# Performance work log

Hardware: AMD Instinct MI355X
Metric: run time of the kernel (lower is better)

The kernel has to match this reference:

```python
import jax, jax.numpy as jnp
import numpy as np
from jax.scipy.special import logsumexp

N_STATES = 512
VOCAB = 10000
BATCH = 64
T_MAX = 1024


def setup_inputs() -> dict:
    key = jax.random.key(0)
    k1, k2, k3, k4, k5 = jax.random.split(key, 5)
    x = jax.random.randint(k1, (BATCH, T_MAX), 0, VOCAB)
    T = jax.random.randint(k2, (BATCH,), 1, T_MAX + 1)  # lengths in [1, T_max]
    priors = jax.random.normal(k3, (N_STATES,), dtype=jnp.float32)
    trans = jax.random.normal(k4, (N_STATES, N_STATES), dtype=jnp.float32)
    emit = jax.random.normal(k5, (N_STATES, VOCAB), dtype=jnp.float32)
    return {"x": x, "T": T, "priors": priors, "trans": trans, "emit": emit}


def reference(x, T, priors, trans, emit):
    # x: (B, Tmax) int, T: (B,) int lengths
    log_pi = jax.nn.log_softmax(priors)            # (N,)
    log_T = jax.nn.log_softmax(trans, axis=0)      # (N, N), columns normalized (dim=0 in torch)
    log_E = jax.nn.log_softmax(emit, axis=1)       # (N, M)

    em = log_E.T[x]                                # (B, Tmax, N) emission log-probs per timestep
    la0 = em[:, 0] + log_pi                        # (B, N)

    def step(la_prev, em_t):
        # out[b, j] = logsumexp_k log_T[j, k] + la_prev[b, k]
        la_new = em_t + logsumexp(log_T[None, :, :] + la_prev[:, None, :], axis=2)
        return la_new, logsumexp(la_new, axis=1)   # carry, per-step log-sum over states

    _, sums = jax.lax.scan(step, la0, jnp.moveaxis(em[:, 1:], 1, 0))  # sums: (Tmax-1, B)
    log_sums = jnp.concatenate([logsumexp(la0, axis=1)[None, :], sums], axis=0)  # (Tmax, B)

    idx = jnp.clip(T, 1, x.shape[1]) - 1           # (B,)
    log_probs = jnp.take_along_axis(log_sums.T, idx[:, None], axis=1)  # (B, 1)
    return log_probs
```

## Files before the change

### kernel.cpp

```cpp
#include <hip/hip_runtime.h>
#include <hip/hip_bf16.h>


typedef unsigned long long u64;
typedef unsigned int u32;
typedef unsigned short u16;
using f32x4 = __attribute__((ext_vector_type(4))) float;
using i32x8 = __attribute__((ext_vector_type(8))) int;

#define N_ST 512
#define VOCAB 10000
#define BATCH 64
#define T_MAX 1024

#define WS_EB       0
#define WS_GB       10240000
#define WS_A8       20480000
#define WS_ROWLSE   20742144
#define WS_COLLSE   20744192
#define WS_PINORM   20746240

static __device__ __forceinline__ float bf16f(u16 h) {
    return __uint_as_float((u32)h << 16);
}
static __device__ __forceinline__ u16 bf16enc(float f) {
    u32 u = __float_as_uint(f);
    return (u16)((u + 0x7fffu + ((u >> 16) & 1u)) >> 16);
}

static __device__ __forceinline__ float dec8(u32 b) {
    float nrm = __uint_as_float((b << 20) + 0x3C000000u);
    float dnm = (float)b * 0x1p-9f;
    return b >= 8u ? nrm : dnm;
}

static __device__ __forceinline__ u32 enc_e4m3(float f) {
    if (!(f > 0.f)) return 0u;
    unsigned u = __float_as_uint(f);
    int e = (int)((u >> 23) & 0xff) - 127;
    unsigned m = u & 0x7fffffu;
    if (e > 8 || (e == 8 && m >= 0x700000u)) return 0x7eu;
    if (e >= -6) {
        unsigned mant = m >> 20;
        unsigned rest = m & 0xfffffu;
        if (rest > 0x80000u || (rest == 0x80000u && (mant & 1u))) mant++;
        unsigned r = ((unsigned)(e + 7) << 3) + mant;
        return r > 0x7eu ? 0x7eu : r;
    }
    if (e < -10) return 0u;
    unsigned full = 0x800000u | m;
    int shift = 23 - (e + 9);
    unsigned r = full >> shift;
    unsigned rem = full & ((1u << shift) - 1u);
    unsigned half = 1u << (shift - 1);
    if (rem > half || (rem == half && (r & 1u))) r++;
    return r;
}

template <bool HI>
static __device__ __forceinline__ u32 cvtpk2(float a, float b, u32 old) {
#if __has_builtin(__builtin_amdgcn_cvt_pk_fp8_f32)
    return (u32)__builtin_amdgcn_cvt_pk_fp8_f32(a, b, (int)old, HI);
#else
    unsigned v = enc_e4m3(a) | (enc_e4m3(b) << 8);
    return HI ? ((old & 0x0000ffffu) | (v << 16)) : ((old & 0xffff0000u) | v);
#endif
}

__global__ __launch_bounds__(256) void k_row_lse(const float* __restrict__ emit,
                                                 float* __restrict__ rowLSE) {
    const int n = blockIdx.x;
    const float* row = emit + (size_t)n * VOCAB;
    __shared__ float redm[4], reds[4];
    const int tid = threadIdx.x, lane = tid & 63, wid = tid >> 6;

    float m = -INFINITY;
    for (int i = tid; i < VOCAB; i += 256) m = fmaxf(m, row[i]);
    #pragma unroll
    for (int o = 32; o; o >>= 1) m = fmaxf(m, __shfl_down(m, o));
    if (lane == 0) redm[wid] = m;
    __syncthreads();
    if (tid == 0) redm[0] = fmaxf(fmaxf(redm[0], redm[1]), fmaxf(redm[2], redm[3]));
    __syncthreads();
    m = redm[0];

    float s = 0.f;
    for (int i = tid; i < VOCAB; i += 256) s += __expf(row[i] - m);
    #pragma unroll
    for (int o = 32; o; o >>= 1) s += __shfl_down(s, o);
    if (lane == 0) reds[wid] = s;
    __syncthreads();
    if (tid == 0) rowLSE[n] = m + __logf(reds[0] + reds[1] + reds[2] + reds[3]);
}

__global__ __launch_bounds__(256) void k_expEmitT(const float* __restrict__ emit,
                                                  const float* __restrict__ rowLSE,
                                                  u16* __restrict__ Eb) {
    const size_t gid = (size_t)blockIdx.x * 256 + threadIdx.x;
    const int m = (int)(gid >> 9);
    const int n = (int)(gid & 511);
    Eb[gid] = bf16enc(__expf(emit[(size_t)n * VOCAB + m] - rowLSE[n]));
}

__global__ __launch_bounds__(256) void k_col_lse(const float* __restrict__ trans,
                                                 float* __restrict__ colLSE) {
    const int k = blockIdx.x;
    const int tid = threadIdx.x, lane = tid & 63, wid = tid >> 6;
    __shared__ float redm[4], reds[4];

    float a = trans[(size_t)tid * N_ST + k];
    float b = trans[(size_t)(tid + 256) * N_ST + k];
    float m = fmaxf(a, b);
    #pragma unroll
    for (int o = 32; o; o >>= 1) m = fmaxf(m, __shfl_down(m, o));
    if (lane == 0) redm[wid] = m;
    __syncthreads();
    if (tid == 0) redm[0] = fmaxf(fmaxf(redm[0], redm[1]), fmaxf(redm[2], redm[3]));
    __syncthreads();
    m = redm[0];

    float s = __expf(a - m) + __expf(b - m);
    #pragma unroll
    for (int o = 32; o; o >>= 1) s += __shfl_down(s, o);
    if (lane == 0) reds[wid] = s;
    __syncthreads();
    if (tid == 0) colLSE[k] = m + __logf(reds[0] + reds[1] + reds[2] + reds[3]);
}

__global__ __launch_bounds__(64) void k_packA_fp8(const float* __restrict__ trans,
                                                  const float* __restrict__ colLSE,
                                                  u32* __restrict__ A8) {
    const int f = blockIdx.x;
    const int l = threadIdx.x;
    const int w = f >> 4, ks = (f >> 2) & 3, jt = f & 3;
    const int j = w * 64 + jt * 16 + (l & 15);
    const int k0 = ks * 128 + (l >> 4) * 32;
    u32 dw[8];
    #pragma unroll
    for (int d = 0; d < 8; ++d) {
        float a0 = 256.0f * __expf(trans[(size_t)j * N_ST + k0 + 4 * d + 0] - colLSE[k0 + 4 * d + 0]);
        float a1 = 256.0f * __expf(trans[(size_t)j * N_ST + k0 + 4 * d + 1] - colLSE[k0 + 4 * d + 1]);
        float a2 = 256.0f * __expf(trans[(size_t)j * N_ST + k0 + 4 * d + 2] - colLSE[k0 + 4 * d + 2]);
        float a3 = 256.0f * __expf(trans[(size_t)j * N_ST + k0 + 4 * d + 3] - colLSE[k0 + 4 * d + 3]);
        u32 pk = cvtpk2<false>(a0, a1, 0u);
        dw[d] = cvtpk2<true>(a2, a3, pk);
    }
    u32* dst = A8 + (size_t)f * 512 + l * 8;
    *(uint4*)dst       = make_uint4(dw[0], dw[1], dw[2], dw[3]);
    *(uint4*)(dst + 4) = make_uint4(dw[4], dw[5], dw[6], dw[7]);
}

__global__ __launch_bounds__(512) void k_pinorm(const float* __restrict__ priors,
                                                float* __restrict__ pinorm) {
    const int j = threadIdx.x, lane = j & 63, wid = j >> 6;
    __shared__ float redm[8], reds[8];
    float v = priors[j];

    float m = v;
    #pragma unroll
    for (int o = 32; o; o >>= 1) m = fmaxf(m, __shfl_down(m, o));
    if (lane == 0) redm[wid] = m;
    __syncthreads();
    if (j == 0) {
        float r = redm[0];
        for (int i = 1; i < 8; ++i) r = fmaxf(r, redm[i]);
        redm[0] = r;
    }
    __syncthreads();
    m = redm[0];

    float s = __expf(v - m);
    #pragma unroll
    for (int o = 32; o; o >>= 1) s += __shfl_down(s, o);
    if (lane == 0) reds[wid] = s;
    __syncthreads();
    if (j == 0) {
        float r = 0.f;
        for (int i = 0; i < 8; ++i) r += reds[i];
        reds[0] = r;
    }
    __syncthreads();
    pinorm[j] = __expf(v - m) / reds[0];
}

__global__ __launch_bounds__(256) void k_G(const u16* __restrict__ Eb,
                                           const float* __restrict__ trans,
                                           const float* __restrict__ colLSE,
                                           u16* __restrict__ Gb) {
    __shared__ float Es[16][512];
    const int m0 = blockIdx.x * 16;
    const int tid = threadIdx.x;
    for (int idx = tid; idx < 16 * 512; idx += 256)
        Es[idx >> 9][idx & 511] = bf16f(Eb[(size_t)(m0 + (idx >> 9)) * 512 + (idx & 511)]);
    __syncthreads();

    const int k0 = tid, k1 = tid + 256;
    const float c0 = colLSE[k0], c1 = colLSE[k1];
    float acc0[16], acc1[16];
    #pragma unroll
    for (int mi = 0; mi < 16; ++mi) { acc0[mi] = 0.f; acc1[mi] = 0.f; }

    for (int j = 0; j < 512; ++j) {
        float a0 = __expf(trans[(size_t)j * N_ST + k0] - c0);
        float a1 = __expf(trans[(size_t)j * N_ST + k1] - c1);
        #pragma unroll
        for (int mi = 0; mi < 16; ++mi) {
            float e = Es[mi][j];
            acc0[mi] = fmaf(e, a0, acc0[mi]);
            acc1[mi] = fmaf(e, a1, acc1[mi]);
        }
    }
    #pragma unroll
    for (int mi = 0; mi < 16; ++mi) {
        Gb[(size_t)(m0 + mi) * N_ST + k0] = bf16enc(acc0[mi]);
        Gb[(size_t)(m0 + mi) * N_ST + k1] = bf16enc(acc1[mi]);
    }
}

#define UNIT_SCALES 0x7f7f7f7f

#define WG_BARRIER()                                        \
  {                                                         \
    asm volatile("s_waitcnt lgkmcnt(0)" ::: "memory");      \
    __builtin_amdgcn_s_barrier();                           \
    asm volatile("" ::: "memory");                          \
  }

#define STEP_BODY(EU, GU, EP, GP)                                               \
  {                                                                             \
    const int xpre = xnext;                                                     \
    GP = *(const uint4*)((const char*)Gb + ((size_t)xpre << 10) + (l << 4));    \
    _Pragma("unroll")                                                           \
    for (int jt = 0; jt < 4; ++jt)                                              \
      EP[jt] = *(const u64*)(Eb + (size_t)xpre * N_ST + wbase + jt * 16 + rbase); \
    xnext = xb[(t + 2 <= Tf) ? (t + 2) : Tf];                                   \
    const u64 vown = vq[p][l];                                                  \
    const u32* vbase = (const u32*)&vq[p][0];                                   \
                                             \
    i32x8 bq[4];                                                                \
    _Pragma("unroll")                                                           \
    for (int ks = 0; ks < 4; ++ks) {                                            \
      const uint4 b0 = *(const uint4*)(vbase + ks * 32 + grp * 8);              \
      const uint4 b1 = *(const uint4*)(vbase + ks * 32 + grp * 8 + 4);          \
      bq[ks] = i32x8{(int)b0.x, (int)b0.y, (int)b0.z, (int)b0.w,                \
                     (int)b1.x, (int)b1.y, (int)b1.z, (int)b1.w};               \
    }                                                                           \
                               \
    f32x4 aA0={0,0,0,0}, aA1={0,0,0,0}, aA2={0,0,0,0}, aA3={0,0,0,0};           \
    f32x4 aB0={0,0,0,0}, aB1={0,0,0,0}, aB2={0,0,0,0}, aB3={0,0,0,0};           \
    _Pragma("unroll")                                                           \
    for (int kk = 0; kk < 2; ++kk) {                                            \
      const int ksA = kk * 2, ksB = kk * 2 + 1;                                 \
      aA0 = __builtin_amdgcn_mfma_scale_f32_16x16x128_f8f6f4(                   \
                af[ksA * 4 + 0], bq[ksA], aA0, 0, 0, 0, UNIT_SCALES, 0, UNIT_SCALES); \
      aB0 = __builtin_amdgcn_mfma_scale_f32_16x16x128_f8f6f4(                   \
                af[ksB * 4 + 0], bq[ksB], aB0, 0, 0, 0, UNIT_SCALES, 0, UNIT_SCALES); \
      aA1 = __builtin_amdgcn_mfma_scale_f32_16x16x128_f8f6f4(                   \
                af[ksA * 4 + 1], bq[ksA], aA1, 0, 0, 0, UNIT_SCALES, 0, UNIT_SCALES); \
      aB1 = __builtin_amdgcn_mfma_scale_f32_16x16x128_f8f6f4(                   \
                af[ksB * 4 + 1], bq[ksB], aB1, 0, 0, 0, UNIT_SCALES, 0, UNIT_SCALES); \
      aA2 = __builtin_amdgcn_mfma_scale_f32_16x16x128_f8f6f4(                   \
                af[ksA * 4 + 2], bq[ksA], aA2, 0, 0, 0, UNIT_SCALES, 0, UNIT_SCALES); \
      aB2 = __builtin_amdgcn_mfma_scale_f32_16x16x128_f8f6f4(                   \
                af[ksB * 4 + 2], bq[ksB], aB2, 0, 0, 0, UNIT_SCALES, 0, UNIT_SCALES); \
      aA3 = __builtin_amdgcn_mfma_scale_f32_16x16x128_f8f6f4(                   \
                af[ksA * 4 + 3], bq[ksA], aA3, 0, 0, 0, UNIT_SCALES, 0, UNIT_SCALES); \
      aB3 = __builtin_amdgcn_mfma_scale_f32_16x16x128_f8f6f4(                   \
                af[ksB * 4 + 3], bq[ksB], aB3, 0, 0, 0, UNIT_SCALES, 0, UNIT_SCALES); \
    }                                                                           \
    float gv = 0.f;                                                             \
    {                                                                           \
      const u32 gw[4] = {GU.x, GU.y, GU.z, GU.w};                               \
      _Pragma("unroll")                                                         \
      for (int i = 0; i < 4; ++i) {                                             \
        float g0 = bf16f((u16)(gw[i] & 0xffffu));                               \
        float g1 = bf16f((u16)(gw[i] >> 16));                                   \
        float v0 = dec8((u32)(vown >> (16 * i)) & 0xffu);                       \
        float v1 = dec8((u32)(vown >> (16 * i + 8)) & 0xffu);                   \
        gv = fmaf(g0, v0, gv);                                                  \
        gv = fmaf(g1, v1, gv);                                                  \
      }                                                                         \
      _Pragma("unroll")                                                         \
      for (int o = 1; o <= 32; o <<= 1) gv += __shfl_xor(gv, o);                \
    }                                                                           \
    float wv2[16];                                                              \
    _Pragma("unroll")                                                           \
    for (int r = 0; r < 4; ++r) {                                               \
      wv2[0 + r]  = bf16f((u16)(EU[0] >> (16 * r))) * (aA0[r] + aB0[r]);        \
      wv2[4 + r]  = bf16f((u16)(EU[1] >> (16 * r))) * (aA1[r] + aB1[r]);        \
      wv2[8 + r]  = bf16f((u16)(EU[2] >> (16 * r))) * (aA2[r] + aB2[r]);        \
      wv2[12 + r] = bf16f((u16)(EU[3] >> (16 * r))) * (aA3[r] + aB3[r]);        \
    }                                                                           \
    if (t == Tf) {                                                              \
      float s2 = 0.f;                                                           \
      _Pragma("unroll")                                                         \
      for (int i = 0; i < 16; ++i) s2 += wv2[i];                                \
      s2 += __shfl_xor(s2, 16);                                                 \
      s2 += __shfl_xor(s2, 32);                                                 \
      if (l == 0) red[wid] = s2;                                                \
      __syncthreads();                                                          \
      const float Se = red[0] + red[1] + red[2] + red[3] +                      \
                       red[4] + red[5] + red[6] + red[7];                       \
      if (tid == 0) out[b] = L + __logf(Se) - (float)Tb * LN256;                \
    } else {                                                                    \
      L += __logf(gv);                                                          \
      const float sc = 1.0f / gv;                                               \
      if ((l & 15) == 0) {                                                      \
        u32* vw = (u32*)&vq[p ^ 1][0];                                          \
        _Pragma("unroll")                                                       \
        for (int jt = 0; jt < 4; ++jt) {                                        \
          u32 pk = cvtpk2<false>(wv2[jt * 4 + 0] * sc, wv2[jt * 4 + 1] * sc, 0u); \
          pk = cvtpk2<true>(wv2[jt * 4 + 2] * sc, wv2[jt * 4 + 3] * sc, pk);    \
          vw[(wbase >> 2) + jt * 4 + grp] = pk;                                 \
        }                                                                       \
      }                                                                         \
      WG_BARRIER();                                                             \
      p ^= 1;                                                                   \
    }                                                                           \
  }

__global__ __launch_bounds__(512, 2) void hmm_main(const int* __restrict__ x,
                                                   const int* __restrict__ T,
                                                   const u16* __restrict__ Eb,
                                                   const u32* __restrict__ A8,
                                                   const u16* __restrict__ Gb,
                                                   const float* __restrict__ pinorm,
                                                   float* __restrict__ out) {
    __shared__ u64 vq[2][64];
    __shared__ float red[8];
    const int b = blockIdx.x;
    const int tid = threadIdx.x;
    const int l = tid & 63;
    const int wid = tid >> 6;
    const int grp = l >> 4;
    const int wbase = wid * 64;
    const int rbase = grp * 4;
    const float LN256 = 5.545177444479562f;

    int Tb = T[b];
    Tb = Tb < 1 ? 1 : (Tb > T_MAX ? T_MAX : Tb);
    const int* xb = x + (size_t)b * T_MAX;

    i32x8 af[16];
    {
        const u32* ap = A8 + (size_t)wid * 16 * 512 + l * 8;
        #pragma unroll
        for (int i = 0; i < 16; ++i) {
            uint4 lo = *(const uint4*)(ap + (size_t)i * 512);
            uint4 hi = *(const uint4*)(ap + (size_t)i * 512 + 4);
            af[i] = i32x8{(int)lo.x, (int)lo.y, (int)lo.z, (int)lo.w,
                          (int)hi.x, (int)hi.y, (int)hi.z, (int)hi.w};
        }
    }

    const int x0 = xb[0];
    const int x1 = xb[1];
    u64 eA[4], eB[4];
    uint4 gA, gB;
    gA = *(const uint4*)((const char*)Gb + ((size_t)x1 << 10) + (l << 4));
    #pragma unroll
    for (int jt = 0; jt < 4; ++jt)
        eA[jt] = *(const u64*)(Eb + (size_t)x1 * N_ST + wbase + jt * 16 + rbase);

    float wv[16];
    float s = 0.f;
    #pragma unroll
    for (int jt = 0; jt < 4; ++jt) {
        u64 eraw = *(const u64*)(Eb + (size_t)x0 * N_ST + wbase + jt * 16 + rbase);
        #pragma unroll
        for (int r = 0; r < 4; ++r) {
            const int j = wbase + jt * 16 + rbase + r;
            float e = bf16f((u16)(eraw >> (16 * r)));
            float t0 = e * pinorm[j];
            wv[jt * 4 + r] = t0;
            s += t0;
        }
    }
    s += __shfl_xor(s, 16);
    s += __shfl_xor(s, 32);
    if (l == 0) red[wid] = s;
    __syncthreads();
    float S0 = red[0] + red[1] + red[2] + red[3] + red[4] + red[5] + red[6] + red[7];
    float L = __logf(S0);
    if (Tb == 1) {
        if (tid == 0) out[b] = L;
        return;
    }
    __syncthreads();
    {
        const float sc = 256.0f / S0;
        if ((l & 15) == 0) {
            u32* vw = (u32*)&vq[0][0];
            #pragma unroll
            for (int jt = 0; jt < 4; ++jt) {
                u32 pk = cvtpk2<false>(wv[jt * 4 + 0] * sc, wv[jt * 4 + 1] * sc, 0u);
                pk = cvtpk2<true>(wv[jt * 4 + 2] * sc, wv[jt * 4 + 3] * sc, pk);
                vw[(wbase >> 2) + jt * 4 + grp] = pk;
            }
        }
    }
    __syncthreads();

    const int Tf = Tb - 1;
    int p = 0;
    int xnext = xb[(2 <= Tf) ? 2 : Tf];
    for (int t = 1;;) {
        STEP_BODY(eA, gA, eB, gB)
        if (t == Tf) break;
        ++t;
        STEP_BODY(eB, gB, eA, gA)
        if (t == Tf) break;
        ++t;
    }
}

extern "C" void kernel_launch(void* const* d_in, const int* in_sizes, int n_in,
                              void* d_out, int out_size, void* d_ws, size_t ws_size,
                              hipStream_t stream) {
    const int*   x      = (const int*)d_in[0];
    const int*   T      = (const int*)d_in[1];
    const float* priors = (const float*)d_in[2];
    const float* trans  = (const float*)d_in[3];
    const float* emit   = (const float*)d_in[4];
    float* out = (float*)d_out;

    char* ws = (char*)d_ws;
    u16*   Eb     = (u16*)(ws + WS_EB);
    u16*   Gb     = (u16*)(ws + WS_GB);
    u32*   A8     = (u32*)(ws + WS_A8);
    float* rowLSE = (float*)(ws + WS_ROWLSE);
    float* colLSE = (float*)(ws + WS_COLLSE);
    float* pinorm = (float*)(ws + WS_PINORM);

    k_row_lse<<<N_ST, 256, 0, stream>>>(emit, rowLSE);
    k_expEmitT<<<(VOCAB * N_ST) / 256, 256, 0, stream>>>(emit, rowLSE, Eb);
    k_col_lse<<<N_ST, 256, 0, stream>>>(trans, colLSE);
    k_packA_fp8<<<128, 64, 0, stream>>>(trans, colLSE, A8);
    k_pinorm<<<1, 512, 0, stream>>>(priors, pinorm);
    k_G<<<VOCAB / 16, 256, 0, stream>>>(Eb, trans, colLSE, Gb);

    hmm_main<<<BATCH, 512, 0, stream>>>(x, T, Eb, A8, Gb, pinorm, out);
}
```

Measured before the change: 1.294 ms.

## Interleave two batch chains per workgroup sharing one barrier per step

Each workgroup now processes two sequences, interleaving their forward-recursion steps so that the MFMA and latency chains of one can overlap the other. Both chains share a single workgroup barrier per timestep, halving the barriers per sequence. The grid is halved to 32 blocks, and the shorter chain idles until the longer one finishes. This lowers parallelism across CUs and raises register pressure.

```diff
diff --git a/kernel.cpp b/kernel.cpp
--- a/kernel.cpp
+++ b/kernel.cpp
@@ -218,6 +218,7 @@
 }
 
 #define UNIT_SCALES 0x7f7f7f7f
+#define LN256 5.545177444479562f
 
 #define WG_BARRIER()                                        \
   {                                                         \
@@ -226,17 +227,16 @@
     asm volatile("" ::: "memory");                          \
   }
 
-#define STEP_BODY(EU, GU, EP, GP)                                               \
-  {                                                                             \
-    const int xpre = xnext;                                                     \
+#define CHAIN_PRE(SUF, EU, GU, EP, GP)                                          \
+  if (t <= Tf##SUF) {                                                           \
+    const int xpre = xnext##SUF;                                                \
     GP = *(const uint4*)((const char*)Gb + ((size_t)xpre << 10) + (l << 4));    \
     _Pragma("unroll")                                                           \
     for (int jt = 0; jt < 4; ++jt)                                              \
       EP[jt] = *(const u64*)(Eb + (size_t)xpre * N_ST + wbase + jt * 16 + rbase); \
-    xnext = xb[(t + 2 <= Tf) ? (t + 2) : Tf];                                   \
-    const u64 vown = vq[p][l];                                                  \
-    const u32* vbase = (const u32*)&vq[p][0];                                   \
-                                             \
+    xnext##SUF = xb##SUF[(t + 2 <= Tf##SUF) ? (t + 2) : Tf##SUF];               \
+    const u64 vown = vq##SUF[p][l];                                             \
+    const u32* vbase = (const u32*)&vq##SUF[p][0];                              \
     i32x8 bq[4];                                                                \
     _Pragma("unroll")                                                           \
     for (int ks = 0; ks < 4; ++ks) {                                            \
@@ -245,7 +245,6 @@
       bq[ks] = i32x8{(int)b0.x, (int)b0.y, (int)b0.z, (int)b0.w,                \
                      (int)b1.x, (int)b1.y, (int)b1.z, (int)b1.w};               \
     }                                                                           \
-                               \
     f32x4 aA0={0,0,0,0}, aA1={0,0,0,0}, aA2={0,0,0,0}, aA3={0,0,0,0};           \
     f32x4 aB0={0,0,0,0}, aB1={0,0,0,0}, aB2={0,0,0,0}, aB3={0,0,0,0};           \
     _Pragma("unroll")                                                           \
@@ -291,22 +290,18 @@
       wv2[8 + r]  = bf16f((u16)(EU[2] >> (16 * r))) * (aA2[r] + aB2[r]);        \
       wv2[12 + r] = bf16f((u16)(EU[3] >> (16 * r))) * (aA3[r] + aB3[r]);        \
     }                                                                           \
-    if (t == Tf) {                                                              \
+    if (t == Tf##SUF) {                                                         \
       float s2 = 0.f;                                                           \
       _Pragma("unroll")                                                         \
       for (int i = 0; i < 16; ++i) s2 += wv2[i];                                \
       s2 += __shfl_xor(s2, 16);                                                 \
       s2 += __shfl_xor(s2, 32);                                                 \
-      if (l == 0) red[wid] = s2;                                                \
-      __syncthreads();                                                          \
-      const float Se = red[0] + red[1] + red[2] + red[3] +                      \
-                       red[4] + red[5] + red[6] + red[7];                       \
-      if (tid == 0) out[b] = L + __logf(Se) - (float)Tb * LN256;                \
+      if (l == 0) redF##SUF[wid] = s2;                                          \
     } else {                                                                    \
-      L += __logf(gv);                                                          \
+      L##SUF += __logf(gv);                                                     \
       const float sc = 1.0f / gv;                                               \
       if ((l & 15) == 0) {                                                      \
-        u32* vw = (u32*)&vq[p ^ 1][0];                                          \
+        u32* vw = (u32*)&vq##SUF[p ^ 1][0];                                     \
         _Pragma("unroll")                                                       \
         for (int jt = 0; jt < 4; ++jt) {                                        \
           u32 pk = cvtpk2<false>(wv2[jt * 4 + 0] * sc, wv2[jt * 4 + 1] * sc, 0u); \
@@ -314,9 +309,23 @@
           vw[(wbase >> 2) + jt * 4 + grp] = pk;                                 \
         }                                                                       \
       }                                                                         \
-      WG_BARRIER();                                                             \
-      p ^= 1;                                                                   \
     }                                                                           \
+  }
+
+#define CHAIN_POST(SUF, CIDX)                                                   \
+  if (t == Tf##SUF && Tb##SUF > 1) {                                            \
+    const float Se = redF##SUF[0] + redF##SUF[1] + redF##SUF[2] + redF##SUF[3] +\
+                     redF##SUF[4] + redF##SUF[5] + redF##SUF[6] + redF##SUF[7]; \
+    if (tid == 0) out[CIDX] = L##SUF + __logf(Se) - (float)Tb##SUF * LN256;     \
+  }
+
+#define ITER(EU0, GU0, EP0, GP0, EU1, GU1, EP1, GP1)                            \
+  {                                                                             \
+    CHAIN_PRE(0, EU0, GU0, EP0, GP0)                                            \
+    CHAIN_PRE(1, EU1, GU1, EP1, GP1)                                            \
+    WG_BARRIER();                                                               \
+    CHAIN_POST(0, c0)                                                           \
+    CHAIN_POST(1, c1)                                                           \
   }
 
 __global__ __launch_bounds__(512, 2) void hmm_main(const int* __restrict__ x,
@@ -326,20 +335,26 @@
                                                    const u16* __restrict__ Gb,
                                                    const float* __restrict__ pinorm,
                                                    float* __restrict__ out) {
-    __shared__ u64 vq[2][64];
-    __shared__ float red[8];
-    const int b = blockIdx.x;
+    __shared__ __align__(16) u64 vq0[2][64];
+    __shared__ __align__(16) u64 vq1[2][64];
+    __shared__ __align__(16) float redF0[8];
+    __shared__ __align__(16) float redF1[8];
+    const int c0 = 2 * blockIdx.x;
+    const int c1 = 2 * blockIdx.x + 1;
     const int tid = threadIdx.x;
     const int l = tid & 63;
     const int wid = tid >> 6;
     const int grp = l >> 4;
     const int wbase = wid * 64;
     const int rbase = grp * 4;
-    const float LN256 = 5.545177444479562f;
-
-    int Tb = T[b];
-    Tb = Tb < 1 ? 1 : (Tb > T_MAX ? T_MAX : Tb);
-    const int* xb = x + (size_t)b * T_MAX;
+
+    int Tb0 = T[c0]; Tb0 = Tb0 < 1 ? 1 : (Tb0 > T_MAX ? T_MAX : Tb0);
+    int Tb1 = T[c1]; Tb1 = Tb1 < 1 ? 1 : (Tb1 > T_MAX ? T_MAX : Tb1);
+    const int* xb0 = x + (size_t)c0 * T_MAX;
+    const int* xb1 = x + (size_t)c1 * T_MAX;
+    const int Tf0 = Tb0 - 1;
+    const int Tf1 = Tb1 - 1;
+    const int Tmax = Tf0 > Tf1 ? Tf0 : Tf1;
 
     i32x8 af[16];
     {
@@ -353,63 +368,84 @@
         }
     }
 
-    const int x0 = xb[0];
-    const int x1 = xb[1];
-    u64 eA[4], eB[4];
-    uint4 gA, gB;
-    gA = *(const uint4*)((const char*)Gb + ((size_t)x1 << 10) + (l << 4));
-    #pragma unroll
-    for (int jt = 0; jt < 4; ++jt)
-        eA[jt] = *(const u64*)(Eb + (size_t)x1 * N_ST + wbase + jt * 16 + rbase);
-
-    float wv[16];
-    float s = 0.f;
-    #pragma unroll
-    for (int jt = 0; jt < 4; ++jt) {
-        u64 eraw = *(const u64*)(Eb + (size_t)x0 * N_ST + wbase + jt * 16 + rbase);
+    u64 eA0[4], eB0[4], eA1[4], eB1[4];
+    uint4 gA0, gB0, gA1, gB1;
+    {
+        const int x10 = xb0[1];
+        const int x11 = xb1[1];
+        gA0 = *(const uint4*)((const char*)Gb + ((size_t)x10 << 10) + (l << 4));
+        gA1 = *(const uint4*)((const char*)Gb + ((size_t)x11 << 10) + (l << 4));
         #pragma unroll
-        for (int r = 0; r < 4; ++r) {
-            const int j = wbase + jt * 16 + rbase + r;
-            float e = bf16f((u16)(eraw >> (16 * r)));
-            float t0 = e * pinorm[j];
-            wv[jt * 4 + r] = t0;
-            s += t0;
+        for (int jt = 0; jt < 4; ++jt) {
+            eA0[jt] = *(const u64*)(Eb + (size_t)x10 * N_ST + wbase + jt * 16 + rbase);
+            eA1[jt] = *(const u64*)(Eb + (size_t)x11 * N_ST + wbase + jt * 16 + rbase);
         }
     }
-    s += __shfl_xor(s, 16);
-    s += __shfl_xor(s, 32);
-    if (l == 0) red[wid] = s;
-    __syncthreads();
-    float S0 = red[0] + red[1] + red[2] + red[3] + red[4] + red[5] + red[6] + red[7];
-    float L = __logf(S0);
-    if (Tb == 1) {
-        if (tid == 0) out[b] = L;
-        return;
-    }
-    __syncthreads();
+
+    float wv_0[16], wv_1[16];
     {
-        const float sc = 256.0f / S0;
+        const int x00 = xb0[0];
+        const int x01 = xb1[0];
+        float s0 = 0.f, s1 = 0.f;
+        #pragma unroll
+        for (int jt = 0; jt < 4; ++jt) {
+            u64 er0 = *(const u64*)(Eb + (size_t)x00 * N_ST + wbase + jt * 16 + rbase);
+            u64 er1 = *(const u64*)(Eb + (size_t)x01 * N_ST + wbase + jt * 16 + rbase);
+            #pragma unroll
+            for (int r = 0; r < 4; ++r) {
+                const int j = wbase + jt * 16 + rbase + r;
+                const float pj = pinorm[j];
+                float t0 = bf16f((u16)(er0 >> (16 * r))) * pj;
+                float t1 = bf16f((u16)(er1 >> (16 * r))) * pj;
+                wv_0[jt * 4 + r] = t0;  s0 += t0;
+                wv_1[jt * 4 + r] = t1;  s1 += t1;
+            }
+        }
+        s0 += __shfl_xor(s0, 16);  s0 += __shfl_xor(s0, 32);
+        s1 += __shfl_xor(s1, 16);  s1 += __shfl_xor(s1, 32);
+        if (l == 0) { redF0[wid] = s0; redF1[wid] = s1; }
+    }
+    __syncthreads();
+    const float S00 = redF0[0] + redF0[1] + redF0[2] + redF0[3] +
+                      redF0[4] + redF0[5] + redF0[6] + redF0[7];
+    const float S01 = redF1[0] + redF1[1] + redF1[2] + redF1[3] +
+                      redF1[4] + redF1[5] + redF1[6] + redF1[7];
+    float L0 = __logf(S00);
+    float L1 = __logf(S01);
+    if (Tb0 == 1 && tid == 0) out[c0] = L0;
+    if (Tb1 == 1 && tid == 0) out[c1] = L1;
+    if (Tmax == 0) return;
+    __syncthreads();
+    {
+        const float sc0 = 256.0f / S00;
+        const float sc1 = 256.0f / S01;
         if ((l & 15) == 0) {
-            u32* vw = (u32*)&vq[0][0];
+            u32* vw0 = (u32*)&vq0[0][0];
+            u32* vw1 = (u32*)&vq1[0][0];
             #pragma unroll
             for (int jt = 0; jt < 4; ++jt) {
-                u32 pk = cvtpk2<false>(wv[jt * 4 + 0] * sc, wv[jt * 4 + 1] * sc, 0u);
-                pk = cvtpk2<true>(wv[jt * 4 + 2] * sc, wv[jt * 4 + 3] * sc, pk);
-                vw[(wbase >> 2) + jt * 4 + grp] = pk;
+                u32 pk0 = cvtpk2<false>(wv_0[jt * 4 + 0] * sc0, wv_0[jt * 4 + 1] * sc0, 0u);
+                pk0 = cvtpk2<true>(wv_0[jt * 4 + 2] * sc0, wv_0[jt * 4 + 3] * sc0, pk0);
+                vw0[(wbase >> 2) + jt * 4 + grp] = pk0;
+                u32 pk1 = cvtpk2<false>(wv_1[jt * 4 + 0] * sc1, wv_1[jt * 4 + 1] * sc1, 0u);
+                pk1 = cvtpk2<true>(wv_1[jt * 4 + 2] * sc1, wv_1[jt * 4 + 3] * sc1, pk1);
+                vw1[(wbase >> 2) + jt * 4 + grp] = pk1;
             }
         }
     }
     __syncthreads();
 
-    const int Tf = Tb - 1;
     int p = 0;
-    int xnext = xb[(2 <= Tf) ? 2 : Tf];
+    int xnext0 = xb0[(2 <= Tf0) ? 2 : Tf0];
+    int xnext1 = xb1[(2 <= Tf1) ? 2 : Tf1];
     for (int t = 1;;) {
-        STEP_BODY(eA, gA, eB, gB)
-        if (t == Tf) break;
+        ITER(eA0, gA0, eB0, gB0, eA1, gA1, eB1, gB1)
+        p ^= 1;
+        if (t == Tmax) break;
         ++t;
-        STEP_BODY(eB, gB, eA, gA)
-        if (t == Tf) break;
+        ITER(eB0, gB0, eA0, gA0, eB1, gB1, eA1, gA1)
+        p ^= 1;
+        if (t == Tmax) break;
         ++t;
     }
 }
@@ -439,5 +475,5 @@
     k_pinorm<<<1, 512, 0, stream>>>(priors, pinorm);
     k_G<<<VOCAB / 16, 256, 0, stream>>>(Eb, trans, colLSE, Gb);
 
-    hmm_main<<<BATCH, 512, 0, stream>>>(x, T, Eb, A8, Gb, pinorm, out);
-}
+    hmm_main<<<BATCH / 2, 512, 0, stream>>>(x, T, Eb, A8, Gb, pinorm, out);
+}
```

After: 2.252 ms. 74.1% more time.

## Split HMM forward step across 16 waves of 32 states each

Applied to the files above, without the earlier changes.

Doubles the workgroup from 8 to 16 waves so each wave owns 32 output states instead of 64. Per-step MFMA work, A-fragment registers and emission loads per wave are halved, and the A8 packing is reorganized to match. This shortens the serial per-timestep critical path in the latency-bound recurrence. The cost is a barrier across twice as many waves, a 16-way reduction, and launch bounds of 1024 with one block per CU.

```diff
diff --git a/kernel.cpp b/kernel.cpp
--- a/kernel.cpp
+++ b/kernel.cpp
@@ -132,8 +132,8 @@
                                                   u32* __restrict__ A8) {
     const int f = blockIdx.x;
     const int l = threadIdx.x;
-    const int w = f >> 4, ks = (f >> 2) & 3, jt = f & 3;
-    const int j = w * 64 + jt * 16 + (l & 15);
+    const int w = f >> 3, ks = (f >> 1) & 3, jt = f & 1;
+    const int j = w * 32 + jt * 16 + (l & 15);
     const int k0 = ks * 128 + (l >> 4) * 32;
     u32 dw[8];
     #pragma unroll
@@ -218,6 +218,7 @@
 }
 
 #define UNIT_SCALES 0x7f7f7f7f
+#define LN256 5.545177444479562f
 
 #define WG_BARRIER()                                        \
   {                                                         \
@@ -231,42 +232,29 @@
     const int xpre = xnext;                                                     \
     GP = *(const uint4*)((const char*)Gb + ((size_t)xpre << 10) + (l << 4));    \
     _Pragma("unroll")                                                           \
-    for (int jt = 0; jt < 4; ++jt)                                              \
+    for (int jt = 0; jt < 2; ++jt)                                              \
       EP[jt] = *(const u64*)(Eb + (size_t)xpre * N_ST + wbase + jt * 16 + rbase); \
     xnext = xb[(t + 2 <= Tf) ? (t + 2) : Tf];                                   \
     const u64 vown = vq[p][l];                                                  \
-    const u32* vbase = (const u32*)&vq[p][0];                                   \
-                                             \
+    const char* vbase = (const char*)&vq[p][0];                                 \
     i32x8 bq[4];                                                                \
     _Pragma("unroll")                                                           \
-    for (int ks = 0; ks < 4; ++ks) {                                            \
-      const uint4 b0 = *(const uint4*)(vbase + ks * 32 + grp * 8);              \
-      const uint4 b1 = *(const uint4*)(vbase + ks * 32 + grp * 8 + 4);          \
-      bq[ks] = i32x8{(int)b0.x, (int)b0.y, (int)b0.z, (int)b0.w,                \
-                     (int)b1.x, (int)b1.y, (int)b1.z, (int)b1.w};               \
+    for (int ks = 0; ks < 4; ++ks)                                              \
+      bq[ks] = *(const i32x8*)(vbase + ks * 128 + grp * 32);                    \
+    f32x4 aA0={0,0,0,0}, aA1={0,0,0,0}, aB0={0,0,0,0}, aB1={0,0,0,0};           \
+    _Pragma("unroll")                                                           \
+    for (int ks = 0; ks < 2; ++ks) {                                            \
+      aA0 = __builtin_amdgcn_mfma_scale_f32_16x16x128_f8f6f4(                   \
+                af[ks * 2 + 0], bq[ks], aA0, 0, 0, 0, UNIT_SCALES, 0, UNIT_SCALES); \
+      aA1 = __builtin_amdgcn_mfma_scale_f32_16x16x128_f8f6f4(                   \
+                af[ks * 2 + 1], bq[ks], aA1, 0, 0, 0, UNIT_SCALES, 0, UNIT_SCALES); \
     }                                                                           \
-                               \
-    f32x4 aA0={0,0,0,0}, aA1={0,0,0,0}, aA2={0,0,0,0}, aA3={0,0,0,0};           \
-    f32x4 aB0={0,0,0,0}, aB1={0,0,0,0}, aB2={0,0,0,0}, aB3={0,0,0,0};           \
     _Pragma("unroll")                                                           \
-    for (int kk = 0; kk < 2; ++kk) {                                            \
-      const int ksA = kk * 2, ksB = kk * 2 + 1;                                 \
-      aA0 = __builtin_amdgcn_mfma_scale_f32_16x16x128_f8f6f4(                   \
-                af[ksA * 4 + 0], bq[ksA], aA0, 0, 0, 0, UNIT_SCALES, 0, UNIT_SCALES); \
+    for (int ks = 2; ks < 4; ++ks) {                                            \
       aB0 = __builtin_amdgcn_mfma_scale_f32_16x16x128_f8f6f4(                   \
-                af[ksB * 4 + 0], bq[ksB], aB0, 0, 0, 0, UNIT_SCALES, 0, UNIT_SCALES); \
-      aA1 = __builtin_amdgcn_mfma_scale_f32_16x16x128_f8f6f4(                   \
-                af[ksA * 4 + 1], bq[ksA], aA1, 0, 0, 0, UNIT_SCALES, 0, UNIT_SCALES); \
+                af[ks * 2 + 0], bq[ks], aB0, 0, 0, 0, UNIT_SCALES, 0, UNIT_SCALES); \
       aB1 = __builtin_amdgcn_mfma_scale_f32_16x16x128_f8f6f4(                   \
-                af[ksB * 4 + 1], bq[ksB], aB1, 0, 0, 0, UNIT_SCALES, 0, UNIT_SCALES); \
-      aA2 = __builtin_amdgcn_mfma_scale_f32_16x16x128_f8f6f4(                   \
-                af[ksA * 4 + 2], bq[ksA], aA2, 0, 0, 0, UNIT_SCALES, 0, UNIT_SCALES); \
-      aB2 = __builtin_amdgcn_mfma_scale_f32_16x16x128_f8f6f4(                   \
-                af[ksB * 4 + 2], bq[ksB], aB2, 0, 0, 0, UNIT_SCALES, 0, UNIT_SCALES); \
-      aA3 = __builtin_amdgcn_mfma_scale_f32_16x16x128_f8f6f4(                   \
-                af[ksA * 4 + 3], bq[ksA], aA3, 0, 0, 0, UNIT_SCALES, 0, UNIT_SCALES); \
-      aB3 = __builtin_amdgcn_mfma_scale_f32_16x16x128_f8f6f4(                   \
-                af[ksB * 4 + 3], bq[ksB], aB3, 0, 0, 0, UNIT_SCALES, 0, UNIT_SCALES); \
+                af[ks * 2 + 1], bq[ks], aB1, 0, 0, 0, UNIT_SCALES, 0, UNIT_SCALES); \
     }                                                                           \
     float gv = 0.f;                                                             \
     {                                                                           \
@@ -283,24 +271,23 @@
       _Pragma("unroll")                                                         \
       for (int o = 1; o <= 32; o <<= 1) gv += __shfl_xor(gv, o);                \
     }                                                                           \
-    float wv2[16];                                                              \
+    float wv2[8];                                                               \
     _Pragma("unroll")                                                           \
     for (int r = 0; r < 4; ++r) {                                               \
-      wv2[0 + r]  = bf16f((u16)(EU[0] >> (16 * r))) * (aA0[r] + aB0[r]);        \
-      wv2[4 + r]  = bf16f((u16)(EU[1] >> (16 * r))) * (aA1[r] + aB1[r]);        \
-      wv2[8 + r]  = bf16f((u16)(EU[2] >> (16 * r))) * (aA2[r] + aB2[r]);        \
-      wv2[12 + r] = bf16f((u16)(EU[3] >> (16 * r))) * (aA3[r] + aB3[r]);        \
+      wv2[0 + r] = bf16f((u16)(EU[0] >> (16 * r))) * (aA0[r] + aB0[r]);         \
+      wv2[4 + r] = bf16f((u16)(EU[1] >> (16 * r))) * (aA1[r] + aB1[r]);         \
     }                                                                           \
     if (t == Tf) {                                                              \
       float s2 = 0.f;                                                           \
       _Pragma("unroll")                                                         \
-      for (int i = 0; i < 16; ++i) s2 += wv2[i];                                \
+      for (int i = 0; i < 8; ++i) s2 += wv2[i];                                 \
       s2 += __shfl_xor(s2, 16);                                                 \
       s2 += __shfl_xor(s2, 32);                                                 \
-      if (l == 0) red[wid] = s2;                                                \
+      if (l == 0) redF[wid] = s2;                                               \
       __syncthreads();                                                          \
-      const float Se = red[0] + red[1] + red[2] + red[3] +                      \
-                       red[4] + red[5] + red[6] + red[7];                       \
+      float Se = 0.f;                                                           \
+      _Pragma("unroll")                                                         \
+      for (int i = 0; i < 16; ++i) Se += redF[i];                               \
       if (tid == 0) out[b] = L + __logf(Se) - (float)Tb * LN256;                \
     } else {                                                                    \
       L += __logf(gv);                                                          \
@@ -308,10 +295,10 @@
       if ((l & 15) == 0) {                                                      \
         u32* vw = (u32*)&vq[p ^ 1][0];                                          \
         _Pragma("unroll")                                                       \
-        for (int jt = 0; jt < 4; ++jt) {                                        \
+        for (int jt = 0; jt < 2; ++jt) {                                        \
           u32 pk = cvtpk2<false>(wv2[jt * 4 + 0] * sc, wv2[jt * 4 + 1] * sc, 0u); \
           pk = cvtpk2<true>(wv2[jt * 4 + 2] * sc, wv2[jt * 4 + 3] * sc, pk);    \
-          vw[(wbase >> 2) + jt * 4 + grp] = pk;                                 \
+          vw[wid * 8 + jt * 4 + grp] = pk;                                      \
         }                                                                       \
       }                                                                         \
       WG_BARRIER();                                                             \
@@ -319,53 +306,48 @@
     }                                                                           \
   }
 
-__global__ __launch_bounds__(512, 2) void hmm_main(const int* __restrict__ x,
-                                                   const int* __restrict__ T,
-                                                   const u16* __restrict__ Eb,
-                                                   const u32* __restrict__ A8,
-                                                   const u16* __restrict__ Gb,
-                                                   const float* __restrict__ pinorm,
-                                                   float* __restrict__ out) {
-    __shared__ u64 vq[2][64];
-    __shared__ float red[8];
+__global__ __launch_bounds__(1024, 1) void hmm_main(const int* __restrict__ x,
+                                                    const int* __restrict__ T,
+                                                    const u16* __restrict__ Eb,
+                                                    const u32* __restrict__ A8,
+                                                    const u16* __restrict__ Gb,
+                                                    const float* __restrict__ pinorm,
+                                                    float* __restrict__ out) {
+    __shared__ __align__(64) u64 vq[2][64];
+    __shared__ __align__(16) float redF[16];
     const int b = blockIdx.x;
     const int tid = threadIdx.x;
     const int l = tid & 63;
     const int wid = tid >> 6;
     const int grp = l >> 4;
-    const int wbase = wid * 64;
+    const int wbase = wid * 32;
     const int rbase = grp * 4;
-    const float LN256 = 5.545177444479562f;
 
     int Tb = T[b];
     Tb = Tb < 1 ? 1 : (Tb > T_MAX ? T_MAX : Tb);
     const int* xb = x + (size_t)b * T_MAX;
 
-    i32x8 af[16];
+    i32x8 af[8];
     {
-        const u32* ap = A8 + (size_t)wid * 16 * 512 + l * 8;
+        const u32* ap = A8 + (size_t)wid * 8 * 512 + l * 8;
         #pragma unroll
-        for (int i = 0; i < 16; ++i) {
-            uint4 lo = *(const uint4*)(ap + (size_t)i * 512);
-            uint4 hi = *(const uint4*)(ap + (size_t)i * 512 + 4);
-            af[i] = i32x8{(int)lo.x, (int)lo.y, (int)lo.z, (int)lo.w,
-                          (int)hi.x, (int)hi.y, (int)hi.z, (int)hi.w};
-        }
+        for (int i = 0; i < 8; ++i)
+            af[i] = *(const i32x8*)(ap + (size_t)i * 512);
     }
 
     const int x0 = xb[0];
     const int x1 = xb[1];
-    u64 eA[4], eB[4];
+    u64 eA[2], eB[2];
     uint4 gA, gB;
     gA = *(const uint4*)((const char*)Gb + ((size_t)x1 << 10) + (l << 4));
     #pragma unroll
-    for (int jt = 0; jt < 4; ++jt)
+    for (int jt = 0; jt < 2; ++jt)
         eA[jt] = *(const u64*)(Eb + (size_t)x1 * N_ST + wbase + jt * 16 + rbase);
 
-    float wv[16];
+    float wv[8];
     float s = 0.f;
     #pragma unroll
-    for (int jt = 0; jt < 4; ++jt) {
+    for (int jt = 0; jt < 2; ++jt) {
         u64 eraw = *(const u64*)(Eb + (size_t)x0 * N_ST + wbase + jt * 16 + rbase);
         #pragma unroll
         for (int r = 0; r < 4; ++r) {
@@ -378,9 +360,11 @@
     }
     s += __shfl_xor(s, 16);
     s += __shfl_xor(s, 32);
-    if (l == 0) red[wid] = s;
-    __syncthreads();
-    float S0 = red[0] + red[1] + red[2] + red[3] + red[4] + red[5] + red[6] + red[7];
+    if (l == 0) redF[wid] = s;
+    __syncthreads();
+    float S0 = 0.f;
+    #pragma unroll
+    for (int i = 0; i < 16; ++i) S0 += redF[i];
     float L = __logf(S0);
     if (Tb == 1) {
         if (tid == 0) out[b] = L;
@@ -392,10 +376,10 @@
         if ((l & 15) == 0) {
             u32* vw = (u32*)&vq[0][0];
             #pragma unroll
-            for (int jt = 0; jt < 4; ++jt) {
+            for (int jt = 0; jt < 2; ++jt) {
                 u32 pk = cvtpk2<false>(wv[jt * 4 + 0] * sc, wv[jt * 4 + 1] * sc, 0u);
                 pk = cvtpk2<true>(wv[jt * 4 + 2] * sc, wv[jt * 4 + 3] * sc, pk);
-                vw[(wbase >> 2) + jt * 4 + grp] = pk;
+                vw[wid * 8 + jt * 4 + grp] = pk;
             }
         }
     }
@@ -439,5 +423,5 @@
     k_pinorm<<<1, 512, 0, stream>>>(priors, pinorm);
     k_G<<<VOCAB / 16, 256, 0, stream>>>(Eb, trans, colLSE, Gb);
 
-    hmm_main<<<BATCH, 512, 0, stream>>>(x, T, Eb, A8, Gb, pinorm, out);
-}
+    hmm_main<<<BATCH, 1024, 0, stream>>>(x, T, Eb, A8, Gb, pinorm, out);
+}
```

After: 2.939 ms. +127.2%, slower.
